# Optimization experiments

Measured on AMD Instinct MI355X. Metric: run time of the kernel, lower is better.

## Reference

```python
import jax, jax.numpy as jnp
import numpy as np

B, L, D_MODEL, D_STATE, D_HIDDEN = 4, 4096, 1024, 256, 4096
RMIN, RMAX, MAX_PHASE = 0.8, 0.95, 2.0 * np.pi


def setup_inputs() -> dict:
    key = jax.random.key(0)
    ks = jax.random.split(key, 10)
    # LRU ring init (Orvieto et al.): |lambda| in [rmin, rmax], phase in [0, max_phase)
    u1 = jax.random.uniform(ks[0], (D_STATE,))
    u2 = jax.random.uniform(ks[1], (D_STATE,))
    nu_log = jnp.log(-0.5 * jnp.log(u1 * (RMAX**2 - RMIN**2) + RMIN**2))
    theta_log = jnp.log(MAX_PHASE * u2)
    B_re = jax.random.normal(ks[2], (D_STATE, D_MODEL)) / np.sqrt(2.0 * D_MODEL)
    B_im = jax.random.normal(ks[3], (D_STATE, D_MODEL)) / np.sqrt(2.0 * D_MODEL)
    C_re = jax.random.normal(ks[4], (D_MODEL, D_STATE)) / np.sqrt(D_STATE)
    C_im = jax.random.normal(ks[5], (D_MODEL, D_STATE)) / np.sqrt(D_STATE)
    D_mat = jax.random.normal(ks[6], (D_MODEL, D_MODEL)) / np.sqrt(D_MODEL)
    W1 = jax.random.normal(ks[7], (D_MODEL, D_HIDDEN)) * np.sqrt(2.0 / D_MODEL)
    W2 = jax.random.normal(ks[8], (D_HIDDEN, D_MODEL)) * np.sqrt(2.0 / D_HIDDEN)
    res_logit = jnp.asarray(-1.0, dtype=jnp.float32)
    x3d = jax.random.normal(ks[9], (B, L, D_MODEL), dtype=jnp.float32)
    return {"x3d": x3d, "nu_log": nu_log, "theta_log": theta_log,
            "B_re": B_re, "B_im": B_im, "C_re": C_re, "C_im": C_im,
            "D_mat": D_mat, "W1": W1, "W2": W2, "res_logit": res_logit}


def _lru_scan(lam, Bu):
    # diagonal linear recurrence x_t = lam * x_{t-1} + Bu_t via associative scan
    lam_b = jnp.broadcast_to(lam, Bu.shape)  # [B, L, N]

    def comb(a, b):
        return (a[0] * b[0], b[0] * a[1] + b[1])

    _, states = jax.lax.associative_scan(comb, (lam_b, Bu), axis=1)
    return states  # [B, L, N] complex


def reference(x3d, nu_log, theta_log, B_re, B_im, C_re, C_im, D_mat, W1, W2, res_logit):
    lam = jnp.exp(-jnp.exp(nu_log) + 1j * jnp.exp(theta_log))          # [N]
    gamma = jnp.sqrt(1.0 - jnp.abs(lam) ** 2)                           # [N]
    Bn = (gamma[:, None] * (B_re + 1j * B_im))                          # [N, D]
    Bu = jnp.einsum('bld,nd->bln', x3d.astype(jnp.complex64), Bn)       # [B, L, N]
    states = _lru_scan(lam.astype(jnp.complex64), Bu)                   # [B, L, N]
    y = jnp.einsum('bln,mn->blm', states, C_re + 1j * C_im).real \
        + jnp.einsum('bld,md->blm', x3d, D_mat)                         # [B, L, D]
    # MLP feedforward (nl_layers=2, bias=False), dropout is identity at p=0
    z = jax.nn.gelu(y @ W1) @ W2                                        # [B, L, D]
    out = x3d + jax.nn.sigmoid(res_logit) * z
    st = states[:, -1]  # final recurrent state
    return out, st
```

## Files before the change

kernel.cpp:

```cpp
#include <hip/hip_runtime.h>
#include <stdint.h>

typedef __bf16 bf16;
typedef bf16 bf16x8 __attribute__((ext_vector_type(8)));
typedef float f32x4 __attribute__((ext_vector_type(4)));

#define B_  4
#define L_  4096
#define DM  1024
#define DS  256
#define DH  4096
#define BL  16384
#define CL  64
#define NC  64

__device__ __forceinline__ float bfbits(uint32_t lo16) {
  union { uint32_t u; float f; } v; v.u = lo16 << 16; return v.f;
}

__device__ __forceinline__ void async16(const bf16* g, bf16* l) {
  __builtin_amdgcn_global_load_lds(
      (const __attribute__((address_space(1))) uint32_t*)g,
      (__attribute__((address_space(3))) uint32_t*)l, 16, 0, 0);
}

#define MEMFENCE()  asm volatile("" ::: "memory")
#define LGKM0()     asm volatile("s_waitcnt lgkmcnt(0)" ::: "memory")
#define MFMA16(a, b, c) __builtin_amdgcn_mfma_f32_16x16x32_bf16((a), (b), (c), 0, 0, 0)
#define SCHEDB()    __builtin_amdgcn_sched_barrier(0)

__global__ void prep_fused(const float4* __restrict__ x, bf16* __restrict__ XS,
                           const float* __restrict__ C_re, const float* __restrict__ C_im,
                           const float* __restrict__ D_mat, bf16* __restrict__ WBy,
                           const float* __restrict__ B_re, const float* __restrict__ B_im,
                           const float* __restrict__ nu_log, const float* __restrict__ th_log,
                           bf16* __restrict__ WBbu,
                           const float* __restrict__ W1, bf16* __restrict__ WB1,
                           const float* __restrict__ W2, bf16* __restrict__ WB2,
                           float* __restrict__ scal) {
  __shared__ float tile[32][33];
  int bid = blockIdx.x, tid = threadIdx.x;
  if (bid < 16384) {
    size_t i = (size_t)bid * 256 + tid;
    size_t t = i >> 8;
    int d4 = (int)(i & 255);
    float4 v = x[i];
    bf16* o = XS + t * 1536 + 512 + (size_t)d4 * 4;
    o[0] = (bf16)v.x; o[1] = (bf16)v.y; o[2] = (bf16)v.z; o[3] = (bf16)v.w;
  } else if (bid < 22528) {
    size_t i = (size_t)(bid - 16384) * 256 + tid;
    int m = (int)(i / 1536), c = (int)(i % 1536);
    float v;
    if (c < 256)       v = C_re[m * 256 + c];
    else if (c < 512)  v = -C_im[m * 256 + (c - 256)];
    else               v = D_mat[m * 1024 + (c - 512)];
    WBy[i] = (bf16)v;
  } else if (bid < 24576) {
    size_t i = (size_t)(bid - 22528) * 256 + tid;
    int row = (int)(i >> 10), col = (int)(i & 1023);
    int n = row >> 1;
    float mod = __expf(-__expf(nu_log[n]));
    float g = sqrtf(fmaxf(1.0f - mod * mod, 0.0f));
    const float* src = (row & 1) ? B_im : B_re;
    WBbu[i] = (bf16)(g * src[n * 1024 + col]);
  } else if (bid < 32768) {
    const float* in; bf16* out; int R, C, bx, by;
    if (bid < 28672) { int t = bid - 24576; in = W1; out = WB1; R = 1024; C = 4096; bx = t & 127; by = t >> 7; }
    else             { int t = bid - 28672; in = W2; out = WB2; R = 4096; C = 1024; bx = t & 31;  by = t >> 5; }
    int c0 = bx * 32, r0 = by * 32, tx = tid & 31, ty = tid >> 5;
    for (int i = 0; i < 32; i += 8)
      tile[ty + i][tx] = in[(size_t)(r0 + ty + i) * C + c0 + tx];
    __syncthreads();
    for (int i = 0; i < 32; i += 8)
      out[(size_t)(c0 + ty + i) * R + r0 + tx] = (bf16)tile[tx][ty + i];
  } else {
    int n = tid;
    float nu = __expf(nu_log[n]);
    float th = __expf(th_log[n]);
    float mod = __expf(-nu);
    float lr = mod * cosf(th);
    float li = mod * sinf(th);
    float g = sqrtf(fmaxf(1.0f - mod * mod, 0.0f));
    float pr = 1.f, pi = 0.f;
    for (int i = 0; i < CL; i++) {
      float nr = pr * lr - pi * li;
      float ni = pr * li + pi * lr;
      pr = nr; pi = ni;
    }
    scal[n] = lr; scal[256 + n] = li;
    scal[512 + n] = pr; scal[768 + n] = pi;
    scal[1024 + n] = g;
  }
}

template <int EPI>
__device__ __forceinline__ void epi_store(void* C, int ldc, size_t row, size_t col,
                                          float v, float sig, const float* xres) {
  size_t off = row * (size_t)ldc + col;
  if (EPI == 0) {
    ((bf16*)C)[off] = (bf16)v;
  } else if (EPI == 1) {
    float z = 0.7978845608f * (v + 0.044715f * v * v * v);
    float gv = v / (1.f + __expf(-2.f * z));
    ((bf16*)C)[off] = (bf16)gv;
  } else {
    ((float*)C)[off] = xres[off] + sig * v;
  }
}

template <int EPI>
__global__ __launch_bounds__(256, 1) void gemm256(
    const bf16* __restrict__ A, int lda,
    const bf16* __restrict__ Bt, int ldb,
    void* __restrict__ C, int ldc, int NK, int mt, int nt,
    const float* __restrict__ xres, const float* __restrict__ reslog) {
  __shared__ __align__(16) bf16 sA[2 * 16384];
  __shared__ __align__(16) bf16 sB[2 * 16384];

  const int tid  = threadIdx.x;
  const int lane = tid & 63;
  const int wave = tid >> 6;
  const int q = lane >> 4, l16 = lane & 15;
  const int wr = wave >> 1, wc = wave & 1;

  int nb = mt * nt;
  int per = nb >> 3;
  int t0 = (blockIdx.x & 7) * per + (blockIdx.x >> 3);
  int gsz = nt << 3;
  int g = t0 / gsz, r = t0 % gsz;
  size_t m0 = (size_t)(g * 8 + (r & 7)) * 256;
  size_t n0 = (size_t)(r >> 3) * 256;

  const int srow = tid >> 3;
  const int scol = (((tid & 7) ^ ((tid >> 3) & 7)) << 3);
  const bf16* gA = A  + (m0 + srow) * (size_t)lda + scol;
  const bf16* gB = Bt + (n0 + srow) * (size_t)ldb + scol;
  bf16* lA = sA + tid * 8;
  bf16* lB = sB + tid * 8;

  auto stageA = [&](int kt) {
    const bf16* s = gA + kt * 64;
    bf16* l = lA + (kt & 1) * 16384;
#pragma unroll
    for (int u = 0; u < 8; ++u)
      async16(s + (size_t)(u * 32) * lda, l + u * 2048);
  };
  auto stageB = [&](int kt) {
    const bf16* s = gB + kt * 64;
    bf16* l = lB + (kt & 1) * 16384;
#pragma unroll
    for (int u = 0; u < 8; ++u)
      async16(s + (size_t)(u * 32) * ldb, l + u * 2048);
  };

  stageA(0); stageB(0);
  __syncthreads();

  const int sw  = (l16 & 7) << 3;
  const int qx0 = (q << 3) ^ sw;
  const int qx1 = ((q << 3) + 32) ^ sw;
  const bf16* Ard = sA + (wr * 128 + l16) * 64;
  const bf16* Brd = sB + (wc * 128 + l16) * 64;

  f32x4 acc[8][8] = {};
  bf16x8 a[8], b[8];

  for (int kt = 0; kt < NK; ++kt) {
    const bf16* Ab = Ard + (kt & 1) * 16384;
    const bf16* Bb = Brd + (kt & 1) * 16384;

#pragma unroll
    for (int m = 0; m < 8; ++m) a[m] = *(const bf16x8*)&Ab[m * 1024 + qx0];
#pragma unroll
    for (int n = 0; n < 8; ++n) b[n] = *(const bf16x8*)&Bb[n * 1024 + qx0];
    if (kt + 1 < NK) stageA(kt + 1);
#pragma unroll
    for (int m = 0; m < 8; ++m)
#pragma unroll
      for (int n = 0; n < 8; ++n)
        acc[m][n] = MFMA16(a[m], b[n], acc[m][n]);

#pragma unroll
    for (int m = 0; m < 8; ++m) a[m] = *(const bf16x8*)&Ab[m * 1024 + qx1];
#pragma unroll
    for (int n = 0; n < 8; ++n) b[n] = *(const bf16x8*)&Bb[n * 1024 + qx1];
    if (kt + 1 < NK) stageB(kt + 1);
#pragma unroll
    for (int m = 0; m < 8; ++m)
#pragma unroll
      for (int n = 0; n < 8; ++n)
        acc[m][n] = MFMA16(a[m], b[n], acc[m][n]);

    __syncthreads();
  }

  float sig = 0.f;
  if (EPI == 2) sig = 1.f / (1.f + __expf(-reslog[0]));
#pragma unroll
  for (int mi = 0; mi < 8; ++mi)
#pragma unroll
    for (int ni = 0; ni < 8; ++ni) {
      size_t col = n0 + wc * 128 + ni * 16 + l16;
#pragma unroll
      for (int r2 = 0; r2 < 4; ++r2) {
        size_t row = m0 + wr * 128 + mi * 16 + q * 4 + r2;
        epi_store<EPI>(C, ldc, row, col, acc[mi][ni][r2], sig, xres);
      }
    }
}

template <int EPI>
__global__ __launch_bounds__(512, 2) void gemm128(
    const bf16* __restrict__ A, int lda,
    const bf16* __restrict__ Bt, int ldb,
    void* __restrict__ C, int ldc, int NK, int mt, int nt,
    const float* __restrict__ xres, const float* __restrict__ reslog) {
  __shared__ __align__(16) bf16 sA[2 * 8192];
  __shared__ __align__(16) bf16 sB[2 * 16384];

  const int tid  = threadIdx.x;
  const int lane = tid & 63;
  const int wave = tid >> 6;
  const int q = lane >> 4, l16 = lane & 15;
  const int wr = wave >> 2, wc = wave & 3;

  int nb = mt * nt;
  int per = nb >> 3;
  int t0 = (blockIdx.x & 7) * per + (blockIdx.x >> 3);
  int gsz = nt << 3;
  int g = t0 / gsz, r = t0 % gsz;
  size_t m0 = (size_t)(g * 8 + (r & 7)) * 128;
  size_t n0 = (size_t)(r >> 3) * 256;

  const int srow = tid >> 3;
  const int scol = (((tid & 7) ^ ((tid >> 3) & 7)) << 3);
  const bf16* gA = A  + (m0 + srow) * (size_t)lda + scol;
  const bf16* gB = Bt + (n0 + srow) * (size_t)ldb + scol;
  bf16* lA = sA + tid * 8;
  bf16* lB = sB + tid * 8;

  auto stageA = [&](int kt) {
    const bf16* s = gA + kt * 64;
    bf16* l = lA + (kt & 1) * 8192;
    async16(s, l);
    async16(s + (size_t)64 * lda, l + 4096);
  };
  auto stageB = [&](int kt) {
    const bf16* s = gB + kt * 64;
    bf16* l = lB + (kt & 1) * 16384;
    async16(s, l);
    async16(s + (size_t)64  * ldb, l + 4096);
    async16(s + (size_t)128 * ldb, l + 8192);
    async16(s + (size_t)192 * ldb, l + 12288);
  };

  stageA(0); stageB(0); stageA(1); stageB(1);
  __builtin_amdgcn_s_waitcnt(0x0F76);
  __builtin_amdgcn_s_barrier();
  MEMFENCE();

  const int sw  = (l16 & 7) << 3;
  const int qx0 = (q << 3) ^ sw;
  const int qx1 = ((q << 3) + 32) ^ sw;
  const bf16* Ard = sA + (wr * 64 + l16) * 64;
  const bf16* Brd = sB + (wc >> 1) * 8192 + ((wc & 1) * 64 + l16) * 64;

  f32x4 acc[4][4] = {};
  bf16x8 a0[4], a1[4], b0[4], b1[4];

#pragma unroll
  for (int j = 0; j < 4; ++j) a0[j] = *(const bf16x8*)&Ard[j * 1024 + qx0];
#pragma unroll
  for (int n = 0; n < 4; ++n) b0[n] = *(const bf16x8*)&Brd[n * 1024 + qx0];

  for (int kt = 0; kt < NK; ++kt) {
    const bf16* Ab  = Ard + (kt & 1) * 8192;
    const bf16* Bb  = Brd + (kt & 1) * 16384;
    const bf16* Abn = Ard + ((kt + 1) & 1) * 8192;
    const bf16* Bbn = Brd + ((kt + 1) & 1) * 16384;

#pragma unroll
    for (int j = 0; j < 4; ++j) a1[j] = *(const bf16x8*)&Ab[j * 1024 + qx1];
#pragma unroll
    for (int n = 0; n < 4; ++n) b1[n] = *(const bf16x8*)&Bb[n * 1024 + qx1];
    SCHEDB();
    __builtin_amdgcn_s_setprio(1);
#pragma unroll
    for (int j = 0; j < 4; ++j)
#pragma unroll
      for (int n = 0; n < 4; ++n)
        acc[j][n] = MFMA16(a0[j], b0[n], acc[j][n]);
    __builtin_amdgcn_s_setprio(0);

    MEMFENCE();
    __builtin_amdgcn_s_waitcnt(0x0F70);
    LGKM0();
    __builtin_amdgcn_s_barrier();
    MEMFENCE();

    if (kt + 1 < NK) {
#pragma unroll
      for (int j = 0; j < 4; ++j) a0[j] = *(const bf16x8*)&Abn[j * 1024 + qx0];
#pragma unroll
      for (int n = 0; n < 4; ++n) b0[n] = *(const bf16x8*)&Bbn[n * 1024 + qx0];
    }
    if (kt + 2 < NK) { stageA(kt + 2); stageB(kt + 2); }
    SCHEDB();
    __builtin_amdgcn_s_setprio(1);
#pragma unroll
    for (int j = 0; j < 4; ++j)
#pragma unroll
      for (int n = 0; n < 4; ++n)
        acc[j][n] = MFMA16(a1[j], b1[n], acc[j][n]);
    __builtin_amdgcn_s_setprio(0);
  }

  float sig = 0.f;
  if (EPI == 2) sig = 1.f / (1.f + __expf(-reslog[0]));
#pragma unroll
  for (int mi = 0; mi < 4; ++mi)
#pragma unroll
    for (int ni = 0; ni < 4; ++ni) {
      size_t col = n0 + wc * 64 + ni * 16 + l16;
#pragma unroll
      for (int r2 = 0; r2 < 4; ++r2) {
        size_t row = m0 + wr * 64 + mi * 16 + q * 4 + r2;
        epi_store<EPI>(C, ldc, row, col, acc[mi][ni][r2], sig, xres);
      }
    }
}

__global__ void scan_pass1(const bf16* __restrict__ Bu, const float* __restrict__ scal,
                           float2* __restrict__ H) {
  int b = blockIdx.x >> 6, c = blockIdx.x & 63, n = threadIdx.x;
  float lr = scal[n], li = scal[256 + n];
  float sr = 0.f, si = 0.f;
  size_t t0 = (size_t)b * L_ + (size_t)c * CL;
  const uint32_t* p = (const uint32_t*)(Bu + t0 * 512) + n;
  for (int j = 0; j < CL; j++) {
    uint32_t u = p[(size_t)j * 256];
    float ur = bfbits(u & 0xffffu), ui = bfbits(u >> 16);
    float nr = lr * sr - li * si + ur;
    float ni = lr * si + li * sr + ui;
    sr = nr; si = ni;
  }
  H[(size_t)(b * NC + c) * 256 + n] = make_float2(sr, si);
}

__global__ void scan_pass2(const float2* __restrict__ H, const float* __restrict__ scal,
                           float2* __restrict__ Carry) {
  int b = blockIdx.x, n = threadIdx.x;
  float Pr = scal[512 + n], Pi = scal[768 + n];
  float cr = 0.f, ci = 0.f;
  for (int c = 0; c < NC; c++) {
    Carry[(size_t)(b * NC + c) * 256 + n] = make_float2(cr, ci);
    float2 h = H[(size_t)(b * NC + c) * 256 + n];
    float nr = Pr * cr - Pi * ci + h.x;
    float ni = Pr * ci + Pi * cr + h.y;
    cr = nr; ci = ni;
  }
}

__global__ void scan_pass3(const bf16* __restrict__ Bu, const float* __restrict__ scal,
                           const float2* __restrict__ Carry, bf16* __restrict__ XS,
                           float* __restrict__ st) {
  int b = blockIdx.x >> 6, c = blockIdx.x & 63, n = threadIdx.x;
  float lr = scal[n], li = scal[256 + n];
  float2 cv = Carry[(size_t)(b * NC + c) * 256 + n];
  float sr = cv.x, si = cv.y;
  size_t t0 = (size_t)b * L_ + (size_t)c * CL;
  const uint32_t* p = (const uint32_t*)(Bu + t0 * 512) + n;
  bf16* qp = XS + t0 * 1536 + n;
  for (int j = 0; j < CL; j++) {
    uint32_t u = p[(size_t)j * 256];
    float ur = bfbits(u & 0xffffu), ui = bfbits(u >> 16);
    float nr = lr * sr - li * si + ur;
    float ni = lr * si + li * sr + ui;
    sr = nr; si = ni;
    qp[(size_t)j * 1536] = (bf16)sr;
    qp[(size_t)j * 1536 + 256] = (bf16)si;
  }
  if (c == NC - 1) {
    st[(size_t)b * 256 + n] = sr;
    st[1024 + (size_t)b * 256 + n] = si;
  }
}

extern "C" void kernel_launch(void* const* d_in, const int* in_sizes, int n_in,
                              void* d_out, int out_size, void* d_ws, size_t ws_size,
                              hipStream_t stream) {
  const float* x      = (const float*)d_in[0];
  const float* nu_log = (const float*)d_in[1];
  const float* th_log = (const float*)d_in[2];
  const float* B_re   = (const float*)d_in[3];
  const float* B_im   = (const float*)d_in[4];
  const float* C_re   = (const float*)d_in[5];
  const float* C_im   = (const float*)d_in[6];
  const float* D_mat  = (const float*)d_in[7];
  const float* W1     = (const float*)d_in[8];
  const float* W2     = (const float*)d_in[9];
  const float* reslog = (const float*)d_in[10];

  char* wsb = (char*)d_ws;
  size_t off = 0;
  auto alloc = [&](size_t bytes) {
    void* p = wsb + off;
    off += (bytes + 255) & ~(size_t)255;
    return p;
  };
  float*  scal = (float*)alloc(5 * 256 * 4);
  bf16*   WBbu = (bf16*)alloc((size_t)512 * 1024 * 2);
  bf16*   WBy  = (bf16*)alloc((size_t)1024 * 1536 * 2);
  bf16*   WB1  = (bf16*)alloc((size_t)4096 * 1024 * 2);
  bf16*   WB2  = (bf16*)alloc((size_t)1024 * 4096 * 2);
  float2* H    = (float2*)alloc((size_t)B_ * NC * 256 * 8);
  float2* Cr   = (float2*)alloc((size_t)B_ * NC * 256 * 8);
  bf16*   Ybf  = (bf16*)alloc((size_t)BL * 1024 * 2);
  bf16*   XS   = (bf16*)alloc((size_t)BL * 1536 * 2);
  bf16*   Bu   = (bf16*)alloc((size_t)BL * 512 * 2);
  bf16*   Hbf  = XS;

  float* out = (float*)d_out;
  float* st  = out + (size_t)BL * DM;

  prep_fused<<<32769, 256, 0, stream>>>(
      (const float4*)x, XS, C_re, C_im, D_mat, WBy,
      B_re, B_im, nu_log, th_log, WBbu, W1, WB1, W2, WB2, scal);

  gemm128<0><<<128 * 2, 512, 0, stream>>>(
      XS + 512, 1536, WBbu, 1024, Bu, 512, 16, 128, 2, nullptr, nullptr);

  scan_pass1<<<B_ * NC, 256, 0, stream>>>(Bu, scal, H);
  scan_pass2<<<B_, 256, 0, stream>>>(H, scal, Cr);
  scan_pass3<<<B_ * NC, 256, 0, stream>>>(Bu, scal, Cr, XS, st);

  gemm256<0><<<64 * 4, 256, 0, stream>>>(
      XS, 1536, WBy, 1536, Ybf, 1024, 24, 64, 4, nullptr, nullptr);

  for (int i = 0; i < 2; i++) {
    const bf16* Yc = Ybf + (size_t)i * 8192 * 1024;
    float* Oc = out + (size_t)i * 8192 * 1024;
    const float* Xc = x + (size_t)i * 8192 * 1024;
    gemm256<1><<<32 * 16, 256, 0, stream>>>(
        Yc, 1024, WB1, 1024, Hbf, 4096, 16, 32, 16, nullptr, nullptr);
    gemm128<2><<<64 * 4, 512, 0, stream>>>(
        Hbf, 4096, WB2, 4096, Oc, 1024, 64, 64, 4, Xc, reslog);
  }
}
```

Before: 642.0 us.

## Restructure gemm256 to 8 waves with single-buffered LDS and explicit barriers

The 256x256 GEMM kernel moves from 4 waves with double-buffered LDS to 8 waves, each computing a 128x64 sub-tile, with single-buffered LDS (64 KB) and launch bounds of 512 threads. Each k-step now waits for the async loads, reads all of its LDS fragments into registers, then barriers before issuing the next global-to-LDS loads, and raises wave priority around the MFMA block. This is meant to cut per-wave register pressure, raise occupancy and let waves overlap the loads for the next tile with MFMA work. In exchange it adds two barriers per k-step and loses explicit double buffering, so load latency may be exposed.

```diff
diff --git a/kernel.cpp b/kernel.cpp
--- a/kernel.cpp
+++ b/kernel.cpp
@@ -109,19 +109,19 @@
 }
 
 template <int EPI>
-__global__ __launch_bounds__(256, 1) void gemm256(
+__global__ __launch_bounds__(512, 4) void gemm256(
     const bf16* __restrict__ A, int lda,
     const bf16* __restrict__ Bt, int ldb,
     void* __restrict__ C, int ldc, int NK, int mt, int nt,
     const float* __restrict__ xres, const float* __restrict__ reslog) {
-  __shared__ __align__(16) bf16 sA[2 * 16384];
-  __shared__ __align__(16) bf16 sB[2 * 16384];
+  __shared__ __align__(16) bf16 sA[16384];
+  __shared__ __align__(16) bf16 sB[16384];
 
   const int tid  = threadIdx.x;
   const int lane = tid & 63;
   const int wave = tid >> 6;
   const int q = lane >> 4, l16 = lane & 15;
-  const int wr = wave >> 1, wc = wave & 1;
+  const int wr = wave >> 2, wc = wave & 3;
 
   int nb = mt * nt;
   int per = nb >> 3;
@@ -140,58 +140,62 @@
 
   auto stageA = [&](int kt) {
     const bf16* s = gA + kt * 64;
-    bf16* l = lA + (kt & 1) * 16384;
-#pragma unroll
-    for (int u = 0; u < 8; ++u)
-      async16(s + (size_t)(u * 32) * lda, l + u * 2048);
+    async16(s, lA);
+    async16(s + (size_t)64  * lda, lA + 4096);
+    async16(s + (size_t)128 * lda, lA + 8192);
+    async16(s + (size_t)192 * lda, lA + 12288);
   };
   auto stageB = [&](int kt) {
     const bf16* s = gB + kt * 64;
-    bf16* l = lB + (kt & 1) * 16384;
-#pragma unroll
-    for (int u = 0; u < 8; ++u)
-      async16(s + (size_t)(u * 32) * ldb, l + u * 2048);
+    async16(s, lB);
+    async16(s + (size_t)64  * ldb, lB + 4096);
+    async16(s + (size_t)128 * ldb, lB + 8192);
+    async16(s + (size_t)192 * ldb, lB + 12288);
   };
 
   stageA(0); stageB(0);
-  __syncthreads();
 
   const int sw  = (l16 & 7) << 3;
   const int qx0 = (q << 3) ^ sw;
   const int qx1 = ((q << 3) + 32) ^ sw;
-  const bf16* Ard = sA + (wr * 128 + l16) * 64;
-  const bf16* Brd = sB + (wc * 128 + l16) * 64;
-
-  f32x4 acc[8][8] = {};
-  bf16x8 a[8], b[8];
+  const bf16* Ard = sA + wr * 8192 + l16 * 64;
+  const bf16* Brd = sB + (wc >> 1) * 8192 + ((wc & 1) * 64 + l16) * 64;
+
+  f32x4 acc[8][4] = {};
+  bf16x8 a[8][2], b[4][2];
 
   for (int kt = 0; kt < NK; ++kt) {
-    const bf16* Ab = Ard + (kt & 1) * 16384;
-    const bf16* Bb = Brd + (kt & 1) * 16384;
-
-#pragma unroll
-    for (int m = 0; m < 8; ++m) a[m] = *(const bf16x8*)&Ab[m * 1024 + qx0];
-#pragma unroll
-    for (int n = 0; n < 8; ++n) b[n] = *(const bf16x8*)&Bb[n * 1024 + qx0];
-    if (kt + 1 < NK) stageA(kt + 1);
-#pragma unroll
-    for (int m = 0; m < 8; ++m)
-#pragma unroll
-      for (int n = 0; n < 8; ++n)
-        acc[m][n] = MFMA16(a[m], b[n], acc[m][n]);
-
-#pragma unroll
-    for (int m = 0; m < 8; ++m) a[m] = *(const bf16x8*)&Ab[m * 1024 + qx1];
-#pragma unroll
-    for (int n = 0; n < 8; ++n) b[n] = *(const bf16x8*)&Bb[n * 1024 + qx1];
-    if (kt + 1 < NK) stageB(kt + 1);
-#pragma unroll
-    for (int m = 0; m < 8; ++m)
-#pragma unroll
-      for (int n = 0; n < 8; ++n)
-        acc[m][n] = MFMA16(a[m], b[n], acc[m][n]);
-
-    __syncthreads();
+    MEMFENCE();
+    __builtin_amdgcn_s_waitcnt(0x0F70);
+    __builtin_amdgcn_s_barrier();
+    MEMFENCE();
+
+#pragma unroll
+    for (int j = 0; j < 8; ++j) {
+      a[j][0] = *(const bf16x8*)&Ard[j * 1024 + qx0];
+      a[j][1] = *(const bf16x8*)&Ard[j * 1024 + qx1];
+    }
+#pragma unroll
+    for (int n = 0; n < 4; ++n) {
+      b[n][0] = *(const bf16x8*)&Brd[n * 1024 + qx0];
+      b[n][1] = *(const bf16x8*)&Brd[n * 1024 + qx1];
+    }
+    LGKM0();
+    MEMFENCE();
+    __builtin_amdgcn_s_barrier();
+    MEMFENCE();
+
+    if (kt + 1 < NK) { stageA(kt + 1); stageB(kt + 1); }
+
+    __builtin_amdgcn_s_setprio(1);
+#pragma unroll
+    for (int j = 0; j < 8; ++j)
+#pragma unroll
+      for (int n = 0; n < 4; ++n) {
+        acc[j][n] = MFMA16(a[j][0], b[n][0], acc[j][n]);
+        acc[j][n] = MFMA16(a[j][1], b[n][1], acc[j][n]);
+      }
+    __builtin_amdgcn_s_setprio(0);
   }
 
   float sig = 0.f;
@@ -199,8 +203,8 @@
 #pragma unroll
   for (int mi = 0; mi < 8; ++mi)
 #pragma unroll
-    for (int ni = 0; ni < 8; ++ni) {
-      size_t col = n0 + wc * 128 + ni * 16 + l16;
+    for (int ni = 0; ni < 4; ++ni) {
+      size_t col = n0 + wc * 64 + ni * 16 + l16;
 #pragma unroll
       for (int r2 = 0; r2 < 4; ++r2) {
         size_t row = m0 + wr * 128 + mi * 16 + q * 4 + r2;
@@ -434,14 +438,14 @@
   scan_pass2<<<B_, 256, 0, stream>>>(H, scal, Cr);
   scan_pass3<<<B_ * NC, 256, 0, stream>>>(Bu, scal, Cr, XS, st);
 
-  gemm256<0><<<64 * 4, 256, 0, stream>>>(
+  gemm256<0><<<64 * 4, 512, 0, stream>>>(
       XS, 1536, WBy, 1536, Ybf, 1024, 24, 64, 4, nullptr, nullptr);
 
   for (int i = 0; i < 2; i++) {
     const bf16* Yc = Ybf + (size_t)i * 8192 * 1024;
     float* Oc = out + (size_t)i * 8192 * 1024;
     const float* Xc = x + (size_t)i * 8192 * 1024;
-    gemm256<1><<<32 * 16, 256, 0, stream>>>(
+    gemm256<1><<<32 * 16, 512, 0, stream>>>(
         Yc, 1024, WB1, 1024, Hbf, 4096, 16, 32, 16, nullptr, nullptr);
     gemm128<2><<<64 * 4, 512, 0, stream>>>(
         Hbf, 4096, WB2, 4096, Oc, 1024, 64, 64, 4, Xc, reslog);
```

Measured after the change: 2.538 ms. 295% more time.
